# Kernel optimization log

Hardware: AMD Instinct MI355X
Metric: run time of the kernel (lower is better)

Reference implementation:

```python
import jax, jax.numpy as jnp
import numpy as np

B, H_IMG, W_IMG = 8, 64, 64
C, HEADS, SR, MSG = 128, 4, 4, 4
N0 = H_IMG * W_IMG


def _linear(x, w, b):
    return x @ w.T + b


def _layernorm(x, g, b, eps=1e-5):
    mu = jnp.mean(x, -1, keepdims=True)
    var = jnp.mean(jnp.square(x - mu), -1, keepdims=True)
    return (x - mu) * jax.lax.rsqrt(var + eps) * g + b


def _conv2d(x, w, b, stride, pad, groups=1):
    y = jax.lax.conv_general_dilated(
        x, w, (stride, stride), [(pad, pad), (pad, pad)],
        dimension_numbers=("NCHW", "OIHW", "NCHW"), feature_group_count=groups)
    return y + b[None, :, None, None]


def setup_inputs():
    key = jax.random.key(0)
    ks = jax.random.split(key, 16)
    def nrm(k, shape, std=0.02):
        return jax.random.normal(k, shape, jnp.float32) * std
    z = lambda *s: jnp.zeros(s, jnp.float32)
    return {
        "x": jax.random.normal(ks[0], (B, N0, C), jnp.float32),
        "msg_tokens": jax.random.normal(ks[1], (B, MSG, C), jnp.float32),
        "Wq": nrm(ks[2], (C, C)), "bq": z(C),
        "sr1_w": nrm(ks[3], (C, C, 4, 4), float(np.sqrt(2.0 / (16 * C)))), "sr1_b": z(C),
        "ln1_g": jnp.ones((C,), jnp.float32), "ln1_b": z(C),
        "sr2_w": nrm(ks[4], (C, C, 2, 2), float(np.sqrt(2.0 / (4 * C)))), "sr2_b": z(C),
        "ln2_g": jnp.ones((C,), jnp.float32), "ln2_b": z(C),
        "kv1_w": nrm(ks[5], (C, C)), "kv1_b": z(C),
        "kv2_w": nrm(ks[6], (C, C)), "kv2_b": z(C),
        "lc1_w": nrm(ks[7], (C // 2, 1, 3, 3), float(np.sqrt(2.0 / 9.0))), "lc1_b": z(C // 2),
        "lc2_w": nrm(ks[8], (C // 2, 1, 3, 3), float(np.sqrt(2.0 / 9.0))), "lc2_b": z(C // 2),
        "proj_w": nrm(ks[9], (C, C)), "proj_b": z(C),
        "H": H_IMG, "W": W_IMG,
    }


def reference(x, msg_tokens, Wq, bq, sr1_w, sr1_b, ln1_g, ln1_b,
              sr2_w, sr2_b, ln2_g, ln2_b, kv1_w, kv1_b, kv2_w, kv2_b,
              lc1_w, lc1_b, lc2_w, lc2_b, proj_w, proj_b, H, W):
    Bsz, _, Cc = x.shape
    m = msg_tokens.shape[1]
    h = HEADS
    dh = Cc // h
    scale = dh ** -0.5
    x_q = jnp.concatenate([x, msg_tokens], axis=1)       # [B, N, C]
    N = x_q.shape[1]
    q = _linear(x_q, Wq, bq).reshape(Bsz, N, h, dh).transpose(0, 2, 1, 3)  # [B,h,N,dh]
    x_img = x.transpose(0, 2, 1).reshape(Bsz, Cc, H, W)

    def branch(sr_w, sr_b, ln_g, ln_b, kv_w, kv_b, lc_w, lc_b, q_half, stride):
        Hr, Wr = H // stride, W // stride
        L = Hr * Wr
        # spatial reduction conv -> tokens
        xr = _conv2d(x_img, sr_w, sr_b, stride, 0).reshape(Bsz, Cc, L).transpose(0, 2, 1)
        # message tokens pass through the SR conv via summed weights
        msg_r = jnp.einsum('bnc,oc->bno', msg_tokens, sr_w.sum((-1, -2))) + sr_b
        xk = jax.nn.gelu(_layernorm(jnp.concatenate([xr, msg_r], 1), ln_g, ln_b), approximate=False)
        kv = _linear(xk, kv_w, kv_b).reshape(Bsz, L + m, 2, h // 2, dh).transpose(2, 0, 3, 1, 4)
        k, v = kv[0], kv[1]                               # [B, h/2, L+m, dh]
        attn = jax.nn.softmax(jnp.einsum('bhnd,bhld->bhnl', q_half, k) * scale, axis=-1)
        # fused depthwise conv on the spatial part of V (message tokens bypass)
        v_flat = v.transpose(0, 2, 1, 3).reshape(Bsz, L + m, Cc // 2).transpose(0, 2, 1)  # [B,C/2,L+m]
        lc = _conv2d(v_flat[:, :, :L].reshape(Bsz, Cc // 2, Hr, Wr), lc_w, lc_b, 1, 1,
                     groups=Cc // 2).reshape(Bsz, Cc // 2, L)
        v_add = jnp.concatenate([lc, v_flat[:, :, L:]], axis=2)
        v = v + v_add.reshape(Bsz, h // 2, dh, L + m).transpose(0, 1, 3, 2)
        return jnp.einsum('bhnl,bhld->bhnd', attn, v).transpose(0, 2, 1, 3).reshape(Bsz, N, Cc // 2)

    x1 = branch(sr1_w, sr1_b, ln1_g, ln1_b, kv1_w, kv1_b, lc1_w, lc1_b, q[:, :h // 2], SR)
    x2 = branch(sr2_w, sr2_b, ln2_g, ln2_b, kv2_w, kv2_b, lc2_w, lc2_b, q[:, h // 2:], SR // 2)
    out = _linear(jnp.concatenate([x1, x2], -1), proj_w, proj_b)
    out = x_q + out                                       # identity = x_q, drop_path = Identity
    return out[:, :-m], out[:, -m:]
```

## Files before the change

### kernel.cpp

```cpp
#include <hip/hip_runtime.h>
#include <math.h>

#define BB 8
#define CC 128
#define N0 4096
#define MSGN 4
#define NTOT 4100
#define IMG 64
#define NPAD 4128
#define QT32 129
#define LMP1 320
#define LMP2 1088

#define OFF_WFQ    0
#define OFF_WFKV1  8192
#define OFF_WFKV2  16384
#define OFF_WFPROJ 24576
#define OFF_WFSR1  32768
#define OFF_WFSR2  163840
#define OFF_QH     196608
#define OFF_XK1    2310144
#define OFF_XK2    2443264
#define OFF_KV1O   2969600
#define OFF_KV2O   3235840
#define OFF_KH1    4288512
#define OFF_VT1    4370432
#define OFF_KH2    4452352
#define OFF_VT2    4730880
#define OFF_XP0    5009408
#define OFF_XP1    7110656
#define OFF_L0     2310144
#define OFF_L1     2441472

typedef _Float16 half8v __attribute__((ext_vector_type(8)));
typedef _Float16 half4v __attribute__((ext_vector_type(4)));
typedef float f32x4 __attribute__((ext_vector_type(4)));

__device__ __forceinline__ size_t af_idx(int m, int k, int Kc) {
    return ((size_t)((m >> 4) * Kc + (k >> 5)) * 64 + ((k >> 3) & 3) * 16 + (m & 15)) * 8 + (k & 7);
}

__device__ __forceinline__ float exp2_fast(float x) {
#if __has_builtin(__builtin_amdgcn_exp2f)
    return __builtin_amdgcn_exp2f(x);
#else
    return __expf(x * 0.6931471805599453f);
#endif
}

__global__ void prep_weights(const float* __restrict__ Wq, const float* __restrict__ kv1,
                             const float* __restrict__ kv2, const float* __restrict__ proj,
                             const float* __restrict__ sr1w, const float* __restrict__ sr2w,
                             float* __restrict__ ws, _Float16* __restrict__ Qh) {
    int u = blockIdx.x * blockDim.x + threadIdx.x;
    if (u >= 49152) {
        int idx = u - 49152;
        if (idx >= BB * 4 * (NPAD - NTOT) * 32) return;
        int d = idx & 31;
        int rest = idx >> 5;
        int n = NTOT + rest % (NPAD - NTOT);
        int rest2 = rest / (NPAD - NTOT);
        int hg = rest2 & 3;
        int b = rest2 >> 2;
        Qh[((size_t)(b * 4 + hg) * NPAD + n) * 32 + d] = (_Float16)0.f;
        return;
    }
    int seg, base;
    const float* w = nullptr;
    _Float16* dst;
    if (u < 2048)        { seg = 0; base = u;          w = Wq;   dst = (_Float16*)(ws + OFF_WFQ); }
    else if (u < 4096)   { seg = 0; base = u - 2048;   w = kv1;  dst = (_Float16*)(ws + OFF_WFKV1); }
    else if (u < 6144)   { seg = 0; base = u - 4096;   w = kv2;  dst = (_Float16*)(ws + OFF_WFKV2); }
    else if (u < 8192)   { seg = 0; base = u - 6144;   w = proj; dst = (_Float16*)(ws + OFF_WFPROJ); }
    else if (u < 40960)  { seg = 1; base = u - 8192;   w = sr1w; dst = (_Float16*)(ws + OFF_WFSR1); }
    else                 { seg = 2; base = u - 40960;  w = sr2w; dst = (_Float16*)(ws + OFF_WFSR2); }
    int lane = base & 63;
    int t = (base >> 6) & 7;
    int kc = base >> 9;
    int n = t * 16 + (lane & 15);
    int k0 = kc * 32 + (lane >> 4) * 8;
    half8v val;
    #pragma unroll
    for (int j = 0; j < 8; ++j) {
        int k = k0 + j;
        float v;
        if (seg == 0) v = w[n * 128 + k];
        else if (seg == 1) v = w[(n * 128 + (k & 127)) * 16 + (k >> 7)];
        else v = w[(n * 128 + (k & 127)) * 4 + (k >> 7)];
        val[j] = (_Float16)v;
    }
    *(half8v*)(dst + (size_t)base * 8) = val;
}

template<int S, int WR, int LL, int LM, int KW>
__device__ __forceinline__ void sr_partial(
    int mtile, int kcbase, int lane, const float* __restrict__ x,
    const float* __restrict__ msg, const _Float16* __restrict__ Wf, f32x4 acc[8]) {
    int m15 = lane & 15, quadk = lane >> 4;
    int m = mtile * 16 + m15;
    bool valid = m < BB * LM;
    const float* base = x;
    bool isimg = false;
    if (valid) {
        int b = m / LM, tok = m - b * LM;
        if (tok < LL) {
            int hr = tok / WR, wr = tok - hr * WR;
            base = x + ((size_t)b * N0 + hr * S * IMG + wr * S) * 128;
            isimg = true;
        } else {
            base = msg + ((size_t)b * MSGN + (tok - LL)) * 128;
        }
    }
    const half8v* Bp = (const half8v*)Wf + lane;
    for (int kk = 0; kk < KW; ++kk) {
        int kc = kcbase + kk;
        int k0 = (kc * 4 + quadk) * 8;
        int c = k0 & 127, ij = k0 >> 7;
        half8v a;
        if (valid) {
            int off;
            if (isimg) {
                int ki = ij / S, kj = ij - ki * S;
                off = (ki * IMG + kj) * 128 + c;
            } else off = c;
            const float4* p4 = (const float4*)(base + off);
            float4 f0 = p4[0], f1 = p4[1];
            a[0] = (_Float16)f0.x; a[1] = (_Float16)f0.y; a[2] = (_Float16)f0.z; a[3] = (_Float16)f0.w;
            a[4] = (_Float16)f1.x; a[5] = (_Float16)f1.y; a[6] = (_Float16)f1.z; a[7] = (_Float16)f1.w;
        } else {
            #pragma unroll
            for (int j = 0; j < 8; ++j) a[j] = (_Float16)0.f;
        }
        #pragma unroll
        for (int t = 0; t < 8; ++t)
            acc[t] = __builtin_amdgcn_mfma_f32_16x16x32_f16(a, Bp[(size_t)(kc * 8 + t) * 64], acc[t], 0, 0, 0);
    }
}

__global__ __launch_bounds__(256) void input_gemms(
    const float* __restrict__ x, const float* __restrict__ msg,
    const _Float16* __restrict__ Wf1, const _Float16* __restrict__ Wf2,
    const float* __restrict__ b1, const float* __restrict__ g1, const float* __restrict__ be1,
    const float* __restrict__ b2, const float* __restrict__ g2, const float* __restrict__ be2,
    _Float16* __restrict__ XK1, _Float16* __restrict__ XK2,
    const _Float16* __restrict__ WfQ, const float* __restrict__ bq,
    _Float16* __restrict__ Qh) {
    __shared__ float red[4][2048];
    int tid = threadIdx.x;
    int lane = tid & 63, wave = tid >> 6;
    int bid = blockIdx.x;

    if (bid >= 646) {
        int mt = (bid - 646) * 4 + wave;
        int m15 = lane & 15, quadk = lane >> 4;
        int m = mt * 16 + m15;
        bool valid = m < BB * NTOT;
        const float* rowp = x;
        if (valid) {
            int b = m / NTOT, n = m - b * NTOT;
            rowp = (n < N0) ? (x + ((size_t)b * N0 + n) * 128)
                            : (msg + ((size_t)b * MSGN + (n - N0)) * 128);
        }
        const half8v* Bp = (const half8v*)WfQ + lane;
        f32x4 acc[8];
        #pragma unroll
        for (int t = 0; t < 8; ++t) acc[t] = (f32x4){0.f, 0.f, 0.f, 0.f};
        #pragma unroll
        for (int kc = 0; kc < 4; ++kc) {
            half8v a;
            if (valid) {
                const float4* p4 = (const float4*)(rowp + (kc * 4 + quadk) * 8);
                float4 f0 = p4[0], f1 = p4[1];
                a[0] = (_Float16)f0.x; a[1] = (_Float16)f0.y; a[2] = (_Float16)f0.z; a[3] = (_Float16)f0.w;
                a[4] = (_Float16)f1.x; a[5] = (_Float16)f1.y; a[6] = (_Float16)f1.z; a[7] = (_Float16)f1.w;
            } else {
                #pragma unroll
                for (int j = 0; j < 8; ++j) a[j] = (_Float16)0.f;
            }
            #pragma unroll
            for (int t = 0; t < 8; ++t)
                acc[t] = __builtin_amdgcn_mfma_f32_16x16x32_f16(a, Bp[(size_t)(kc * 8 + t) * 64], acc[t], 0, 0, 0);
        }
        int quad = lane >> 4, n15 = lane & 15;
        const float qscale = 0.17677669529663687f * 1.4426950408889634f;
        #pragma unroll
        for (int r = 0; r < 4; ++r) {
            int mm = mt * 16 + quad * 4 + r;
            if (mm >= BB * NTOT) continue;
            int b = mm / NTOT, tok = mm - b * NTOT;
            #pragma unroll
            for (int t = 0; t < 8; ++t) {
                int n = t * 16 + n15;
                Qh[((size_t)(b * 4 + (n >> 5)) * NPAD + tok) * 32 + (n & 31)] =
                    (_Float16)((acc[t][r] + bq[n]) * qscale);
            }
        }
        return;
    }

    f32x4 acc[8];
    #pragma unroll
    for (int t = 0; t < 8; ++t) acc[t] = (f32x4){0.f, 0.f, 0.f, 0.f};
    const float* bias;
    const float* lng;
    const float* lnb;
    _Float16* outp;
    int mtile, Mv;
    if (bid < 132) {
        mtile = bid; Mv = 2080;
        sr_partial<4, 16, 256, 260, 16>(mtile, wave * 16, lane, x, msg, Wf1, acc);
        bias = b1; lng = g1; lnb = be1; outp = XK1;
    } else {
        mtile = bid - 132; Mv = 8224;
        sr_partial<2, 32, 1024, 1028, 4>(mtile, wave * 4, lane, x, msg, Wf2, acc);
        bias = b2; lng = g2; lnb = be2; outp = XK2;
    }
    int quad = lane >> 4, n15 = lane & 15;
    #pragma unroll
    for (int t = 0; t < 8; ++t)
        #pragma unroll
        for (int r = 0; r < 4; ++r)
            red[wave][(quad * 4 + r) * 128 + t * 16 + n15] = acc[t][r];
    __syncthreads();
    for (int e = tid; e < 2048; e += 256)
        red[0][e] = red[0][e] + red[1][e] + red[2][e] + red[3][e];
    __syncthreads();
    int r16 = tid >> 4, l16 = tid & 15;
    int m = mtile * 16 + r16;
    float v[8];
    float s = 0.f;
    #pragma unroll
    for (int j = 0; j < 8; ++j) { v[j] = red[0][r16 * 128 + j * 16 + l16] + bias[j * 16 + l16]; s += v[j]; }
    #pragma unroll
    for (int off = 1; off < 16; off <<= 1) s += __shfl_xor(s, off);
    float mu = s * (1.f / 128.f);
    float q = 0.f;
    #pragma unroll
    for (int j = 0; j < 8; ++j) { v[j] -= mu; q += v[j] * v[j]; }
    #pragma unroll
    for (int off = 1; off < 16; off <<= 1) q += __shfl_xor(q, off);
    float rs = rsqrtf(q * (1.f / 128.f) + 1e-5f);
    if (m < Mv) {
        #pragma unroll
        for (int j = 0; j < 8; ++j) {
            int n = j * 16 + l16;
            float y = v[j] * rs * lng[n] + lnb[n];
            y = 0.5f * y * (1.f + erff(y * 0.70710678118654752f));
            outp[af_idx(m, n, 4)] = (_Float16)y;
        }
    }
}

__global__ __launch_bounds__(256) void kv_gemm(
    const _Float16* __restrict__ XK1, const _Float16* __restrict__ XK2,
    const _Float16* __restrict__ Wf1, const _Float16* __restrict__ Wf2,
    const float* __restrict__ b1, const float* __restrict__ b2,
    float* __restrict__ o1, float* __restrict__ o2) {
    int lane = threadIdx.x & 63, wave = threadIdx.x >> 6;
    int t = blockIdx.x * 4 + wave;
    int lt;
    const half8v* Ap;
    const half8v* Bp;
    const float* bias;
    float* outp;
    if (t < 130) { lt = t;       Ap = (const half8v*)XK1 + (size_t)lt * 4 * 64 + lane; Bp = (const half8v*)Wf1 + lane; bias = b1; outp = o1; }
    else         { lt = t - 130; Ap = (const half8v*)XK2 + (size_t)lt * 4 * 64 + lane; Bp = (const half8v*)Wf2 + lane; bias = b2; outp = o2; }
    f32x4 acc[8];
    #pragma unroll
    for (int tt = 0; tt < 8; ++tt) acc[tt] = (f32x4){0.f, 0.f, 0.f, 0.f};
    #pragma unroll
    for (int kc = 0; kc < 4; ++kc) {
        half8v a = Ap[(size_t)kc * 64];
        #pragma unroll
        for (int tt = 0; tt < 8; ++tt)
            acc[tt] = __builtin_amdgcn_mfma_f32_16x16x32_f16(a, Bp[(size_t)(kc * 8 + tt) * 64], acc[tt], 0, 0, 0);
    }
    int quad = lane >> 4, n15 = lane & 15;
    #pragma unroll
    for (int r = 0; r < 4; ++r) {
        int m = lt * 16 + quad * 4 + r;
        #pragma unroll
        for (int tt = 0; tt < 8; ++tt)
            outp[(size_t)m * 128 + tt * 16 + n15] = acc[tt][r] + bias[tt * 16 + n15];
    }
}

__global__ void pack_kv(const float* __restrict__ kv1o, const float* __restrict__ kv2o,
                        const float* __restrict__ lc1w, const float* __restrict__ lc1b,
                        const float* __restrict__ lc2w, const float* __restrict__ lc2b,
                        _Float16* __restrict__ Kh1, _Float16* __restrict__ Vt1,
                        _Float16* __restrict__ Kh2, _Float16* __restrict__ Vt2) {
    int idx = blockIdx.x * 256 + threadIdx.x;
    const int T1 = BB * LMP1 * 64;
    const float* kv;
    const float* lcw;
    const float* lcb;
    _Float16* Kh;
    _Float16* Vt;
    int Wr, L, Lm, Lmp, li;
    if (idx < T1) { li = idx;      kv = kv1o; lcw = lc1w; lcb = lc1b; Kh = Kh1; Vt = Vt1; Wr = 16; L = 256;  Lm = 260;  Lmp = LMP1; }
    else          { li = idx - T1; kv = kv2o; lcw = lc2w; lcb = lc2b; Kh = Kh2; Vt = Vt2; Wr = 32; L = 1024; Lm = 1028; Lmp = LMP2; }
    int ch = li & 63;
    int rest = li >> 6;
    int n = rest % Lmp;
    int b = rest / Lmp;
    int h2 = ch >> 5, d = ch & 31;
    int Hr = L / Wr;
    float kval = 0.f, vnew = 0.f;
    if (n < Lm) {
        const float* kvb = kv + (size_t)b * Lm * 128;
        kval = kvb[(size_t)n * 128 + ch];
        float v = kvb[(size_t)n * 128 + 64 + ch];
        float add;
        if (n < L) {
            int hr = n / Wr, wr = n - hr * Wr;
            float sum = lcb[ch];
            #pragma unroll
            for (int ki = 0; ki < 3; ++ki)
                #pragma unroll
                for (int kj = 0; kj < 3; ++kj) {
                    int y = hr + ki - 1, xx = wr + kj - 1;
                    if ((unsigned)y < (unsigned)Hr && (unsigned)xx < (unsigned)Wr)
                        sum += lcw[ch * 9 + ki * 3 + kj] * kvb[((size_t)y * Wr + xx) * 128 + 64 + ch];
                }
            add = sum;
        } else {
            add = v;
        }
        vnew = v + add;
    }
    Kh[((size_t)(b * 2 + h2) * Lmp + n) * 32 + d] = (_Float16)kval;
    Vt[(size_t)(b * 2 + h2) * Lmp * 32 + (size_t)(n >> 2) * 128
       + (d & 15) * 8 + ((d >> 4) << 2) + (n & 3)] = (_Float16)vnew;
}

__global__ __launch_bounds__(256, 4) void attn_mfma(
    const _Float16* __restrict__ Qh,
    const _Float16* __restrict__ Kh1, const _Float16* __restrict__ Vt1,
    const _Float16* __restrict__ Kh2, const _Float16* __restrict__ Vt2,
    _Float16* __restrict__ XP0, _Float16* __restrict__ XP1,
    float* __restrict__ L0, float* __restrict__ L1) {
    int tid = threadIdx.x;
    int lane = tid & 63, wave = tid >> 6;
    int b = blockIdx.y;
    int z = blockIdx.z;
    int h2 = z & 1, h = z >> 1;
    int tile = blockIdx.x * 4 + wave;
    if (tile >= QT32) return;
    int n0 = tile * 32;
    int q16 = lane & 15, quad = lane >> 4;
    const f32x4 zf = {0.f, 0.f, 0.f, 0.f};
    _Float16* xp = h ? XP1 : XP0;
    float* Lp = h ? L1 : L0;

    for (int br = 0; br < 2; ++br) {
        int Lmp = br ? LMP2 : LMP1;
        int k_lo = h ? (br ? 576 : 192) : 0;
        int k_hi = br ? (h ? 1088 : 576) : (h ? 320 : 192);
        const _Float16* kb = (br ? Kh2 : Kh1) + (size_t)(b * 2 + h2) * Lmp * 32;
        const _Float16* vb = (br ? Vt2 : Vt1) + (size_t)(b * 2 + h2) * Lmp * 32;
        int hg = br * 2 + h2;
        const _Float16* qp = Qh + ((size_t)(b * 4 + hg) * NPAD + n0 + q16) * 32 + quad * 8;
        half8v qf0 = *(const half8v*)qp;
        half8v qf1 = *(const half8v*)(qp + 512);
        f32x4 O00 = zf, O01 = zf, O10 = zf, O11 = zf;
        float la = 0.f, lb = 0.f;

        half8v kf[4];
        #pragma unroll
        for (int i = 0; i < 4; ++i)
            kf[i] = *(const half8v*)(kb + (size_t)(k_lo + i * 16 + q16) * 32 + quad * 8);

        for (int k0 = k_lo; k0 < k_hi; k0 += 64) {
            half8v vv[4];
            #pragma unroll
            for (int i = 0; i < 4; ++i)
                vv[i] = *(const half8v*)(vb + (size_t)((k0 >> 2) + i * 4 + quad) * 128 + q16 * 8);
            int k0n = (k0 + 64 < k_hi) ? k0 + 64 : k_lo;
            half8v kn[4];
            #pragma unroll
            for (int i = 0; i < 4; ++i)
                kn[i] = *(const half8v*)(kb + (size_t)(k0n + i * 16 + q16) * 32 + quad * 8);

            half4v p0[4], p1[4];
            #pragma unroll
            for (int i = 0; i < 4; ++i) {
                f32x4 s0 = __builtin_amdgcn_mfma_f32_16x16x32_f16(kf[i], qf0, zf, 0, 0, 0);
                f32x4 s1 = __builtin_amdgcn_mfma_f32_16x16x32_f16(kf[i], qf1, zf, 0, 0, 0);
                half4v a, c;
                #pragma unroll
                for (int r = 0; r < 4; ++r) {
                    float e0 = exp2_fast(s0[r]); la += e0; a[r] = (_Float16)e0;
                    float e1 = exp2_fast(s1[r]); lb += e1; c[r] = (_Float16)e1;
                }
                p0[i] = a; p1[i] = c;
            }
            #pragma unroll
            for (int i = 0; i < 4; ++i) {
                half4v v0 = __builtin_shufflevector(vv[i], vv[i], 0, 1, 2, 3);
                half4v v1 = __builtin_shufflevector(vv[i], vv[i], 4, 5, 6, 7);
                O00 = __builtin_amdgcn_mfma_f32_16x16x16f16(p0[i], v0, O00, 0, 0, 0);
                O01 = __builtin_amdgcn_mfma_f32_16x16x16f16(p0[i], v1, O01, 0, 0, 0);
                O10 = __builtin_amdgcn_mfma_f32_16x16x16f16(p1[i], v0, O10, 0, 0, 0);
                O11 = __builtin_amdgcn_mfma_f32_16x16x16f16(p1[i], v1, O11, 0, 0, 0);
            }
            #pragma unroll
            for (int i = 0; i < 4; ++i) kf[i] = kn[i];
        }

        la += __shfl_xor(la, 16); la += __shfl_xor(la, 32);
        lb += __shfl_xor(lb, 16); lb += __shfl_xor(lb, 32);
        if (h) { la -= 60.0f; lb -= 60.0f; }
        if (quad == 0) {
            int na = n0 + q16;
            if (na < NTOT) Lp[(size_t)(b * NTOT + na) * 4 + hg] = la;
            int nb = n0 + 16 + q16;
            if (nb < NTOT) Lp[(size_t)(b * NTOT + nb) * 4 + hg] = lb;
        }
        int kbase = br * 64 + h2 * 32;
        #pragma unroll
        for (int r = 0; r < 4; ++r) {
            int n = n0 + quad * 4 + r;
            if (n < NTOT) {
                int m = b * NTOT + n;
                xp[af_idx(m, kbase + q16, 4)] = (_Float16)O00[r];
                xp[af_idx(m, kbase + 16 + q16, 4)] = (_Float16)O01[r];
            }
            int n2 = n + 16;
            if (n2 < NTOT) {
                int m = b * NTOT + n2;
                xp[af_idx(m, kbase + q16, 4)] = (_Float16)O10[r];
                xp[af_idx(m, kbase + 16 + q16, 4)] = (_Float16)O11[r];
            }
        }
    }
}

__global__ __launch_bounds__(256) void proj_gemm(
    const _Float16* __restrict__ XP0, const _Float16* __restrict__ XP1,
    const float* __restrict__ L0, const float* __restrict__ L1,
    const _Float16* __restrict__ Wf, const float* __restrict__ bias,
    float* __restrict__ out_f32, const float* __restrict__ x, const float* __restrict__ msg) {
    int lane = threadIdx.x & 63, wave = threadIdx.x >> 6;
    int mt = blockIdx.x * 4 + wave;
    const half8v* Ap0 = (const half8v*)XP0 + (size_t)mt * 4 * 64 + lane;
    const half8v* Ap1 = (const half8v*)XP1 + (size_t)mt * 4 * 64 + lane;
    const half8v* Bp = (const half8v*)Wf + lane;
    int m15 = lane & 15;
    int mrow = mt * 16 + m15;
    bool lvalid = mrow < BB * NTOT;
    f32x4 acc[8];
    #pragma unroll
    for (int t = 0; t < 8; ++t) acc[t] = (f32x4){0.f, 0.f, 0.f, 0.f};
    #pragma unroll
    for (int kc = 0; kc < 4; ++kc) {
        half8v a0 = Ap0[(size_t)kc * 64];
        half8v a1 = Ap1[(size_t)kc * 64];
        float inv = 0.f;
        if (lvalid) {
            float l0 = L0[(size_t)mrow * 4 + kc];
            float l1 = L1[(size_t)mrow * 4 + kc];
            inv = 1.f / (l0 + l1);
        }
        half8v a;
        #pragma unroll
        for (int j = 0; j < 8; ++j)
            a[j] = (_Float16)(((float)a0[j] + (float)a1[j]) * inv);
        #pragma unroll
        for (int t = 0; t < 8; ++t)
            acc[t] = __builtin_amdgcn_mfma_f32_16x16x32_f16(a, Bp[(size_t)(kc * 8 + t) * 64], acc[t], 0, 0, 0);
    }
    int quad = lane >> 4, n15 = lane & 15;
    #pragma unroll
    for (int r = 0; r < 4; ++r) {
        int m = mt * 16 + quad * 4 + r;
        if (m >= BB * NTOT) continue;
        int b = m / NTOT, tok = m - b * NTOT;
        const float* rp;
        float* dst;
        if (tok < N0) {
            rp = x + ((size_t)b * N0 + tok) * 128;
            dst = out_f32 + ((size_t)b * N0 + tok) * 128;
        } else {
            rp = msg + ((size_t)b * MSGN + (tok - N0)) * 128;
            dst = out_f32 + (size_t)BB * N0 * 128 + ((size_t)b * MSGN + (tok - N0)) * 128;
        }
        #pragma unroll
        for (int t = 0; t < 8; ++t) {
            int n = t * 16 + n15;
            dst[n] = acc[t][r] + bias[n] + rp[n];
        }
    }
}

extern "C" void kernel_launch(void* const* d_in, const int* in_sizes, int n_in,
                              void* d_out, int out_size, void* d_ws, size_t ws_size,
                              hipStream_t stream) {
    const float* x     = (const float*)d_in[0];
    const float* msg   = (const float*)d_in[1];
    const float* Wq    = (const float*)d_in[2];
    const float* bq    = (const float*)d_in[3];
    const float* sr1w  = (const float*)d_in[4];
    const float* sr1b  = (const float*)d_in[5];
    const float* ln1g  = (const float*)d_in[6];
    const float* ln1b  = (const float*)d_in[7];
    const float* sr2w  = (const float*)d_in[8];
    const float* sr2b  = (const float*)d_in[9];
    const float* ln2g  = (const float*)d_in[10];
    const float* ln2b  = (const float*)d_in[11];
    const float* kv1w  = (const float*)d_in[12];
    const float* kv1b  = (const float*)d_in[13];
    const float* kv2w  = (const float*)d_in[14];
    const float* kv2b  = (const float*)d_in[15];
    const float* lc1w  = (const float*)d_in[16];
    const float* lc1b  = (const float*)d_in[17];
    const float* lc2w  = (const float*)d_in[18];
    const float* lc2b  = (const float*)d_in[19];
    const float* projw = (const float*)d_in[20];
    const float* projb = (const float*)d_in[21];
    float* ws  = (float*)d_ws;
    float* out = (float*)d_out;

    _Float16* WfQ    = (_Float16*)(ws + OFF_WFQ);
    _Float16* WfKV1  = (_Float16*)(ws + OFF_WFKV1);
    _Float16* WfKV2  = (_Float16*)(ws + OFF_WFKV2);
    _Float16* WfPROJ = (_Float16*)(ws + OFF_WFPROJ);
    _Float16* WfSR1  = (_Float16*)(ws + OFF_WFSR1);
    _Float16* WfSR2  = (_Float16*)(ws + OFF_WFSR2);
    _Float16* Qh     = (_Float16*)(ws + OFF_QH);
    _Float16* XP0    = (_Float16*)(ws + OFF_XP0);
    _Float16* XP1    = (_Float16*)(ws + OFF_XP1);
    float* L0        = ws + OFF_L0;
    float* L1        = ws + OFF_L1;
    _Float16* XK1    = (_Float16*)(ws + OFF_XK1);
    _Float16* XK2    = (_Float16*)(ws + OFF_XK2);
    float* kv1o      = ws + OFF_KV1O;
    float* kv2o      = ws + OFF_KV2O;
    _Float16* Kh1    = (_Float16*)(ws + OFF_KH1);
    _Float16* Vt1    = (_Float16*)(ws + OFF_VT1);
    _Float16* Kh2    = (_Float16*)(ws + OFF_KH2);
    _Float16* Vt2    = (_Float16*)(ws + OFF_VT2);

    prep_weights<<<304, 256, 0, stream>>>(Wq, kv1w, kv2w, projw, sr1w, sr2w, ws, Qh);
    input_gemms<<<1159, 256, 0, stream>>>(x, msg, WfSR1, WfSR2,
                                          sr1b, ln1g, ln1b, sr2b, ln2g, ln2b,
                                          XK1, XK2, WfQ, bq, Qh);
    kv_gemm<<<161, 256, 0, stream>>>(XK1, XK2, WfKV1, WfKV2, kv1b, kv2b, kv1o, kv2o);
    pack_kv<<<2816, 256, 0, stream>>>(kv1o, kv2o, lc1w, lc1b, lc2w, lc2b,
                                      Kh1, Vt1, Kh2, Vt2);
    attn_mfma<<<dim3(33, 8, 4), 256, 0, stream>>>(Qh, Kh1, Vt1, Kh2, Vt2,
                                                  XP0, XP1, L0, L1);
    proj_gemm<<<513, 256, 0, stream>>>(XP0, XP1, L0, L1, WfPROJ, projb, out, x, msg);
}
```

Before: 209.8 us.

## Give each attention block a whole branch and normalize in-kernel instead of split-K

Previously each attention block walked both branches, with the key range split into two halves across blocks. Two partial outputs and row sums were written out and merged and normalized inside the projection GEMM. Now each block handles one branch over its full key range and normalizes by the row sum before writing a single output buffer. The projection GEMM then reads one operand with no L buffers or reciprocal. This removes the duplicate XP buffer traffic and the merge work, at the cost of unbalanced work between the short and long branches. Blocks shrink to two waves and the grid grows to match, and Q padding and the prep grid change to fit.

```diff
diff --git a/kernel.cpp b/kernel.cpp
--- a/kernel.cpp
+++ b/kernel.cpp
@@ -7,8 +7,7 @@
 #define MSGN 4
 #define NTOT 4100
 #define IMG 64
-#define NPAD 4128
-#define QT32 129
+#define NPAD 4160
 #define LMP1 320
 #define LMP2 1088
 
@@ -19,18 +18,15 @@
 #define OFF_WFSR1  32768
 #define OFF_WFSR2  163840
 #define OFF_QH     196608
-#define OFF_XK1    2310144
-#define OFF_XK2    2443264
-#define OFF_KV1O   2969600
-#define OFF_KV2O   3235840
-#define OFF_KH1    4288512
-#define OFF_VT1    4370432
-#define OFF_KH2    4452352
-#define OFF_VT2    4730880
-#define OFF_XP0    5009408
-#define OFF_XP1    7110656
-#define OFF_L0     2310144
-#define OFF_L1     2441472
+#define OFF_XK1    2326528
+#define OFF_XK2    2459648
+#define OFF_KV1O   2985984
+#define OFF_KV2O   3252224
+#define OFF_KH1    4304896
+#define OFF_VT1    4386816
+#define OFF_KH2    4468736
+#define OFF_VT2    4747264
+#define OFF_XP     5025792
 
 typedef _Float16 half8v __attribute__((ext_vector_type(8)));
 typedef _Float16 half4v __attribute__((ext_vector_type(4)));
@@ -334,138 +330,115 @@
        + (d & 15) * 8 + ((d >> 4) << 2) + (n & 3)] = (_Float16)vnew;
 }
 
-__global__ __launch_bounds__(256, 4) void attn_mfma(
+__global__ __launch_bounds__(128, 8) void attn_mfma(
     const _Float16* __restrict__ Qh,
     const _Float16* __restrict__ Kh1, const _Float16* __restrict__ Vt1,
     const _Float16* __restrict__ Kh2, const _Float16* __restrict__ Vt2,
-    _Float16* __restrict__ XP0, _Float16* __restrict__ XP1,
-    float* __restrict__ L0, float* __restrict__ L1) {
+    _Float16* __restrict__ XP) {
     int tid = threadIdx.x;
     int lane = tid & 63, wave = tid >> 6;
     int b = blockIdx.y;
     int z = blockIdx.z;
-    int h2 = z & 1, h = z >> 1;
-    int tile = blockIdx.x * 4 + wave;
-    if (tile >= QT32) return;
+    int h2 = z & 1, br = 1 - (z >> 1);
+    int tile = blockIdx.x * 2 + wave;
     int n0 = tile * 32;
     int q16 = lane & 15, quad = lane >> 4;
     const f32x4 zf = {0.f, 0.f, 0.f, 0.f};
-    _Float16* xp = h ? XP1 : XP0;
-    float* Lp = h ? L1 : L0;
-
-    for (int br = 0; br < 2; ++br) {
-        int Lmp = br ? LMP2 : LMP1;
-        int k_lo = h ? (br ? 576 : 192) : 0;
-        int k_hi = br ? (h ? 1088 : 576) : (h ? 320 : 192);
-        const _Float16* kb = (br ? Kh2 : Kh1) + (size_t)(b * 2 + h2) * Lmp * 32;
-        const _Float16* vb = (br ? Vt2 : Vt1) + (size_t)(b * 2 + h2) * Lmp * 32;
-        int hg = br * 2 + h2;
-        const _Float16* qp = Qh + ((size_t)(b * 4 + hg) * NPAD + n0 + q16) * 32 + quad * 8;
-        half8v qf0 = *(const half8v*)qp;
-        half8v qf1 = *(const half8v*)(qp + 512);
-        f32x4 O00 = zf, O01 = zf, O10 = zf, O11 = zf;
-        float la = 0.f, lb = 0.f;
-
-        half8v kf[4];
+    int Lmp  = br ? LMP2 : LMP1;
+    int k_hi = Lmp;
+    const _Float16* kb = (br ? Kh2 : Kh1) + (size_t)(b * 2 + h2) * Lmp * 32;
+    const _Float16* vb = (br ? Vt2 : Vt1) + (size_t)(b * 2 + h2) * Lmp * 32;
+    int hg = br * 2 + h2;
+    const _Float16* qp = Qh + ((size_t)(b * 4 + hg) * NPAD + n0 + q16) * 32 + quad * 8;
+    half8v qf0 = *(const half8v*)qp;
+    half8v qf1 = *(const half8v*)(qp + 512);
+    f32x4 O00 = zf, O01 = zf, O10 = zf, O11 = zf;
+    float la = 0.f, lb = 0.f;
+
+    half8v kf[4];
+    #pragma unroll
+    for (int i = 0; i < 4; ++i)
+        kf[i] = *(const half8v*)(kb + (size_t)(i * 16 + q16) * 32 + quad * 8);
+
+    for (int k0 = 0; k0 < k_hi; k0 += 64) {
+        half8v vv[4];
         #pragma unroll
         for (int i = 0; i < 4; ++i)
-            kf[i] = *(const half8v*)(kb + (size_t)(k_lo + i * 16 + q16) * 32 + quad * 8);
-
-        for (int k0 = k_lo; k0 < k_hi; k0 += 64) {
-            half8v vv[4];
+            vv[i] = *(const half8v*)(vb + (size_t)((k0 >> 2) + i * 4 + quad) * 128 + q16 * 8);
+        int k0n = (k0 + 64 < k_hi) ? k0 + 64 : 0;
+        half8v kn[4];
+        #pragma unroll
+        for (int i = 0; i < 4; ++i)
+            kn[i] = *(const half8v*)(kb + (size_t)(k0n + i * 16 + q16) * 32 + quad * 8);
+
+        half4v p0[4], p1[4];
+        #pragma unroll
+        for (int i = 0; i < 4; ++i) {
+            f32x4 s0 = __builtin_amdgcn_mfma_f32_16x16x32_f16(kf[i], qf0, zf, 0, 0, 0);
+            f32x4 s1 = __builtin_amdgcn_mfma_f32_16x16x32_f16(kf[i], qf1, zf, 0, 0, 0);
+            half4v a, c;
             #pragma unroll
-            for (int i = 0; i < 4; ++i)
-                vv[i] = *(const half8v*)(vb + (size_t)((k0 >> 2) + i * 4 + quad) * 128 + q16 * 8);
-            int k0n = (k0 + 64 < k_hi) ? k0 + 64 : k_lo;
-            half8v kn[4];
-            #pragma unroll
-            for (int i = 0; i < 4; ++i)
-                kn[i] = *(const half8v*)(kb + (size_t)(k0n + i * 16 + q16) * 32 + quad * 8);
-
-            half4v p0[4], p1[4];
-            #pragma unroll
-            for (int i = 0; i < 4; ++i) {
-                f32x4 s0 = __builtin_amdgcn_mfma_f32_16x16x32_f16(kf[i], qf0, zf, 0, 0, 0);
-                f32x4 s1 = __builtin_amdgcn_mfma_f32_16x16x32_f16(kf[i], qf1, zf, 0, 0, 0);
-                half4v a, c;
-                #pragma unroll
-                for (int r = 0; r < 4; ++r) {
-                    float e0 = exp2_fast(s0[r]); la += e0; a[r] = (_Float16)e0;
-                    float e1 = exp2_fast(s1[r]); lb += e1; c[r] = (_Float16)e1;
-                }
-                p0[i] = a; p1[i] = c;
+            for (int r = 0; r < 4; ++r) {
+                float e0 = exp2_fast(s0[r]); la += e0; a[r] = (_Float16)e0;
+                float e1 = exp2_fast(s1[r]); lb += e1; c[r] = (_Float16)e1;
             }
-            #pragma unroll
-            for (int i = 0; i < 4; ++i) {
-                half4v v0 = __builtin_shufflevector(vv[i], vv[i], 0, 1, 2, 3);
-                half4v v1 = __builtin_shufflevector(vv[i], vv[i], 4, 5, 6, 7);
-                O00 = __builtin_amdgcn_mfma_f32_16x16x16f16(p0[i], v0, O00, 0, 0, 0);
-                O01 = __builtin_amdgcn_mfma_f32_16x16x16f16(p0[i], v1, O01, 0, 0, 0);
-                O10 = __builtin_amdgcn_mfma_f32_16x16x16f16(p1[i], v0, O10, 0, 0, 0);
-                O11 = __builtin_amdgcn_mfma_f32_16x16x16f16(p1[i], v1, O11, 0, 0, 0);
-            }
-            #pragma unroll
-            for (int i = 0; i < 4; ++i) kf[i] = kn[i];
-        }
-
-        la += __shfl_xor(la, 16); la += __shfl_xor(la, 32);
-        lb += __shfl_xor(lb, 16); lb += __shfl_xor(lb, 32);
-        if (h) { la -= 60.0f; lb -= 60.0f; }
-        if (quad == 0) {
-            int na = n0 + q16;
-            if (na < NTOT) Lp[(size_t)(b * NTOT + na) * 4 + hg] = la;
-            int nb = n0 + 16 + q16;
-            if (nb < NTOT) Lp[(size_t)(b * NTOT + nb) * 4 + hg] = lb;
-        }
-        int kbase = br * 64 + h2 * 32;
-        #pragma unroll
-        for (int r = 0; r < 4; ++r) {
-            int n = n0 + quad * 4 + r;
-            if (n < NTOT) {
-                int m = b * NTOT + n;
-                xp[af_idx(m, kbase + q16, 4)] = (_Float16)O00[r];
-                xp[af_idx(m, kbase + 16 + q16, 4)] = (_Float16)O01[r];
-            }
-            int n2 = n + 16;
-            if (n2 < NTOT) {
-                int m = b * NTOT + n2;
-                xp[af_idx(m, kbase + q16, 4)] = (_Float16)O10[r];
-                xp[af_idx(m, kbase + 16 + q16, 4)] = (_Float16)O11[r];
-            }
+            p0[i] = a; p1[i] = c;
+        }
+        #pragma unroll
+        for (int i = 0; i < 4; ++i) {
+            half4v v0 = __builtin_shufflevector(vv[i], vv[i], 0, 1, 2, 3);
+            half4v v1 = __builtin_shufflevector(vv[i], vv[i], 4, 5, 6, 7);
+            O00 = __builtin_amdgcn_mfma_f32_16x16x16f16(p0[i], v0, O00, 0, 0, 0);
+            O01 = __builtin_amdgcn_mfma_f32_16x16x16f16(p0[i], v1, O01, 0, 0, 0);
+            O10 = __builtin_amdgcn_mfma_f32_16x16x16f16(p1[i], v0, O10, 0, 0, 0);
+            O11 = __builtin_amdgcn_mfma_f32_16x16x16f16(p1[i], v1, O11, 0, 0, 0);
+        }
+        #pragma unroll
+        for (int i = 0; i < 4; ++i) kf[i] = kn[i];
+    }
+
+    la += __shfl_xor(la, 16); la += __shfl_xor(la, 32);
+    lb += __shfl_xor(lb, 16); lb += __shfl_xor(lb, 32);
+    la -= 60.0f; lb -= 60.0f;
+    float ia = 1.0f / la;
+    float ib = 1.0f / lb;
+
+    int kbase = br * 64 + h2 * 32;
+    #pragma unroll
+    for (int r = 0; r < 4; ++r) {
+        int row = quad * 4 + r;
+        int src = (lane & 48) | row;
+        float fa = __shfl(ia, src);
+        float fb = __shfl(ib, src);
+        int n = n0 + row;
+        if (n < NTOT) {
+            int m = b * NTOT + n;
+            XP[af_idx(m, kbase + q16, 4)] = (_Float16)(O00[r] * fa);
+            XP[af_idx(m, kbase + 16 + q16, 4)] = (_Float16)(O01[r] * fa);
+        }
+        int n2 = n + 16;
+        if (n2 < NTOT) {
+            int m = b * NTOT + n2;
+            XP[af_idx(m, kbase + q16, 4)] = (_Float16)(O10[r] * fb);
+            XP[af_idx(m, kbase + 16 + q16, 4)] = (_Float16)(O11[r] * fb);
         }
     }
 }
 
 __global__ __launch_bounds__(256) void proj_gemm(
-    const _Float16* __restrict__ XP0, const _Float16* __restrict__ XP1,
-    const float* __restrict__ L0, const float* __restrict__ L1,
+    const _Float16* __restrict__ XP,
     const _Float16* __restrict__ Wf, const float* __restrict__ bias,
     float* __restrict__ out_f32, const float* __restrict__ x, const float* __restrict__ msg) {
     int lane = threadIdx.x & 63, wave = threadIdx.x >> 6;
     int mt = blockIdx.x * 4 + wave;
-    const half8v* Ap0 = (const half8v*)XP0 + (size_t)mt * 4 * 64 + lane;
-    const half8v* Ap1 = (const half8v*)XP1 + (size_t)mt * 4 * 64 + lane;
+    const half8v* Ap = (const half8v*)XP + (size_t)mt * 4 * 64 + lane;
     const half8v* Bp = (const half8v*)Wf + lane;
-    int m15 = lane & 15;
-    int mrow = mt * 16 + m15;
-    bool lvalid = mrow < BB * NTOT;
     f32x4 acc[8];
     #pragma unroll
     for (int t = 0; t < 8; ++t) acc[t] = (f32x4){0.f, 0.f, 0.f, 0.f};
     #pragma unroll
     for (int kc = 0; kc < 4; ++kc) {
-        half8v a0 = Ap0[(size_t)kc * 64];
-        half8v a1 = Ap1[(size_t)kc * 64];
-        float inv = 0.f;
-        if (lvalid) {
-            float l0 = L0[(size_t)mrow * 4 + kc];
-            float l1 = L1[(size_t)mrow * 4 + kc];
-            inv = 1.f / (l0 + l1);
-        }
-        half8v a;
-        #pragma unroll
-        for (int j = 0; j < 8; ++j)
-            a[j] = (_Float16)(((float)a0[j] + (float)a1[j]) * inv);
+        half8v a = Ap[(size_t)kc * 64];
         #pragma unroll
         for (int t = 0; t < 8; ++t)
             acc[t] = __builtin_amdgcn_mfma_f32_16x16x32_f16(a, Bp[(size_t)(kc * 8 + t) * 64], acc[t], 0, 0, 0);
@@ -528,10 +501,7 @@
     _Float16* WfSR1  = (_Float16*)(ws + OFF_WFSR1);
     _Float16* WfSR2  = (_Float16*)(ws + OFF_WFSR2);
     _Float16* Qh     = (_Float16*)(ws + OFF_QH);
-    _Float16* XP0    = (_Float16*)(ws + OFF_XP0);
-    _Float16* XP1    = (_Float16*)(ws + OFF_XP1);
-    float* L0        = ws + OFF_L0;
-    float* L1        = ws + OFF_L1;
+    _Float16* XP     = (_Float16*)(ws + OFF_XP);
     _Float16* XK1    = (_Float16*)(ws + OFF_XK1);
     _Float16* XK2    = (_Float16*)(ws + OFF_XK2);
     float* kv1o      = ws + OFF_KV1O;
@@ -541,14 +511,13 @@
     _Float16* Kh2    = (_Float16*)(ws + OFF_KH2);
     _Float16* Vt2    = (_Float16*)(ws + OFF_VT2);
 
-    prep_weights<<<304, 256, 0, stream>>>(Wq, kv1w, kv2w, projw, sr1w, sr2w, ws, Qh);
+    prep_weights<<<432, 256, 0, stream>>>(Wq, kv1w, kv2w, projw, sr1w, sr2w, ws, Qh);
     input_gemms<<<1159, 256, 0, stream>>>(x, msg, WfSR1, WfSR2,
                                           sr1b, ln1g, ln1b, sr2b, ln2g, ln2b,
                                           XK1, XK2, WfQ, bq, Qh);
     kv_gemm<<<161, 256, 0, stream>>>(XK1, XK2, WfKV1, WfKV2, kv1b, kv2b, kv1o, kv2o);
     pack_kv<<<2816, 256, 0, stream>>>(kv1o, kv2o, lc1w, lc1b, lc2w, lc2b,
                                       Kh1, Vt1, Kh2, Vt2);
-    attn_mfma<<<dim3(33, 8, 4), 256, 0, stream>>>(Qh, Kh1, Vt1, Kh2, Vt2,
-                                                  XP0, XP1, L0, L1);
-    proj_gemm<<<513, 256, 0, stream>>>(XP0, XP1, L0, L1, WfPROJ, projb, out, x, msg);
-}
+    attn_mfma<<<dim3(65, 8, 4), 128, 0, stream>>>(Qh, Kh1, Vt1, Kh2, Vt2, XP);
+    proj_gemm<<<513, 256, 0, stream>>>(XP, WfPROJ, projb, out, x, msg);
+}
```

Result: slower. 226.1 us (+7.8%).
